# Optimization experiments

Hardware: AMD Instinct MI355X
Metric: run time of the kernel (lower is better)

Reference implementation:

```python
import jax, jax.numpy as jnp
import numpy as np

B_, L, DM = 2, 2048, 1024
DI, N, K, R = 2048, 16, 4, 64  # d_inner, d_state, d_conv, dt_rank


def setup_inputs() -> dict:
    key = jax.random.key(0)
    ks = jax.random.split(key, 8)
    return {
        "x": jax.random.normal(ks[0], (B_, L, DM), jnp.float32),
        "W_in": jax.random.normal(ks[1], (DM, 2 * DI), jnp.float32) * 0.02,
        "w_conv": jax.random.normal(ks[2], (DI, K), jnp.float32) * 0.1,
        "b_conv": jnp.zeros((DI,), jnp.float32),
        "W_x": jax.random.normal(ks[3], (DI, R + 2 * N), jnp.float32) * 0.02,
        "W_dt": jax.random.normal(ks[4], (R, DI), jnp.float32) * 0.02,
        "b_dt": jnp.full((DI,), -4.6, jnp.float32),  # softplus(b_dt) ~ 0.01 dt init
        "A_log": jnp.log(jnp.broadcast_to(jnp.arange(1, N + 1, dtype=jnp.float32), (DI, N))),
        "D": jnp.ones((DI,), jnp.float32),
        "W_out": jax.random.normal(ks[5], (DI, DM), jnp.float32) * 0.02,
        "gamma": jnp.ones((DM,), jnp.float32),
        "beta": jnp.zeros((DM,), jnp.float32),
    }


def reference(x, W_in, w_conv, b_conv, W_x, W_dt, b_dt, A_log, D, W_out, gamma, beta):
    Bb, Ll, Dm = x.shape
    Di, Kk = w_conv.shape
    Nn = A_log.shape[1]
    Rr = W_dt.shape[0]
    # in_proj -> (u, z)
    xz = x @ W_in  # [B,L,2*Di]
    u, z = jnp.split(xz, 2, axis=-1)
    # depthwise causal conv1d (kernel K, left pad K-1) + SiLU
    up = jnp.pad(u, ((0, 0), (Kk - 1, 0), (0, 0)))
    conv = b_conv + sum(up[:, k:k + Ll, :] * w_conv[:, k] for k in range(Kk))
    u = jax.nn.silu(conv)  # [B,L,Di]
    # x_proj -> dt, B, C
    dbc = u @ W_x
    dt, Bm, Cm = dbc[..., :Rr], dbc[..., Rr:Rr + Nn], dbc[..., Rr + Nn:]
    delta = jax.nn.softplus(dt @ W_dt + b_dt)  # [B,L,Di]
    A = -jnp.exp(A_log)  # [Di,N]

    def step(h, inputs):
        d_t, B_t, C_t, u_t = inputs  # [B,Di],[B,N],[B,N],[B,Di]
        dA = jnp.exp(d_t[..., None] * A)            # [B,Di,N]
        h = h * dA + (d_t * u_t)[..., None] * B_t[:, None, :]
        y = jnp.einsum('bdn,bn->bd', h, C_t)
        return h, y

    h0 = jnp.zeros((Bb, Di, Nn), x.dtype)
    _, ys = jax.lax.scan(step, h0, (delta.transpose(1, 0, 2), Bm.transpose(1, 0, 2),
                                    Cm.transpose(1, 0, 2), u.transpose(1, 0, 2)))
    y = ys.transpose(1, 0, 2)        # [B,L,Di]
    y = y + u * D                    # skip term
    y = y * jax.nn.silu(z)           # gate
    out = y @ W_out                  # [B,L,Dm]
    # LayerNorm
    mu = out.mean(-1, keepdims=True)
    var = ((out - mu) ** 2).mean(-1, keepdims=True)
    out = (out - mu) * jax.lax.rsqrt(var + 1e-5) * gamma + beta
    # dropout p=0 -> identity; residual
    return out + x
```

## Files before the change

### kernel.cpp

```cpp
#include <hip/hip_runtime.h>
#include <math.h>

#define L_SEQ 2048
#define DMOD  1024
#define DIN   2048
#define NBATCH 2
#define NTOK  (NBATCH * L_SEQ)
#define NST   16
#define RRANK 64
#define LOG2E 1.44269504088896f

#define GCHUNK 64
#define CLEN   (L_SEQ / GCHUNK)
#define SCHUNK 8
#define NSTAGE (CLEN / SCHUNK)

#define G4_KS   4
#define G4_KC   (2048 / G4_KS)
#define G2_KS   16
#define G2_KC   (2048 / G2_KS)

typedef __attribute__((ext_vector_type(8))) short  short8;
typedef __attribute__((ext_vector_type(4))) float  f32x4;

__device__ __forceinline__ ushort f2bf(float f) {
    unsigned u = __float_as_uint(f);
    u += 0x7fffu + ((u >> 16) & 1u);
    return (ushort)(u >> 16);
}
__device__ __forceinline__ float bf2f(ushort u) {
    return __uint_as_float(((unsigned)u) << 16);
}
__device__ __forceinline__ float fexp2(float x) {
    return __builtin_amdgcn_exp2f(x);
}

__device__ __forceinline__ void gload16(const ushort* g, ushort* l) {
    __builtin_amdgcn_global_load_lds(
        (const __attribute__((address_space(1))) unsigned int*)g,
        (__attribute__((address_space(3))) unsigned int*)l,
        16, 0, 0);
}

__device__ __forceinline__ void cast_body(
    const float* __restrict__ src, ushort* __restrict__ dst, int bid, int tid)
{
    int i = (bid * 256 + tid) * 8;
    float4 a = *(const float4*)(src + i);
    float4 b = *(const float4*)(src + i + 4);
    ushort4 o0 = make_ushort4(f2bf(a.x), f2bf(a.y), f2bf(a.z), f2bf(a.w));
    ushort4 o1 = make_ushort4(f2bf(b.x), f2bf(b.y), f2bf(b.z), f2bf(b.w));
    *(ushort4*)(dst + i)     = o0;
    *(ushort4*)(dst + i + 4) = o1;
}

__device__ __forceinline__ void tcast_body(
    const float* __restrict__ src, ushort* __restrict__ dst,
    int R, int C, int bx, int by, int tid)
{
    __shared__ float t[32][33];
    int tx = tid & 31;
    int ty = tid >> 5;
    int c0 = bx * 32;
    int r0 = by * 32;
    #pragma unroll
    for (int i = 0; i < 4; ++i)
        t[ty + i * 8][tx] = src[(size_t)(r0 + ty + i * 8) * C + c0 + tx];
    __syncthreads();
    #pragma unroll
    for (int i = 0; i < 4; ++i)
        dst[(size_t)(c0 + ty + i * 8) * R + r0 + tx] = f2bf(t[tx][ty + i * 8]);
}

__global__ __launch_bounds__(256) void prep_k(
    const float* __restrict__ x, const float* __restrict__ W_in,
    const float* __restrict__ W_dt, const float* __restrict__ W_x,
    const float* __restrict__ W_out,
    ushort* __restrict__ xb, ushort* __restrict__ Wib,
    ushort* __restrict__ Wdtb, ushort* __restrict__ Wxb,
    ushort* __restrict__ Wob)
{
    int bid = blockIdx.x, tid = threadIdx.x;
    if (bid < 2048) {
        cast_body(x, xb, bid, tid);
    } else if (bid < 6144) {
        int t = bid - 2048;
        tcast_body(W_in, Wib, 1024, 4096, t & 127, t >> 7, tid);
    } else if (bid < 6272) {
        int t = bid - 6144;
        tcast_body(W_dt, Wdtb, 64, 2048, t & 63, t >> 6, tid);
    } else if (bid < 6464) {
        int t = bid - 6272;
        tcast_body(W_x, Wxb, 2048, 96, t % 3, t / 3, tid);
    } else {
        int t = bid - 6464;
        tcast_body(W_out, Wob, 2048, 1024, t & 31, t >> 5, tid);
    }
}

__global__ __launch_bounds__(512, 2) void gemm8p(
    const ushort* __restrict__ A,
    const ushort* __restrict__ Bt,
    ushort* __restrict__ C,
    int K, int kslice, int ldc, size_t zstride)
{
    __shared__ ushort lds[65536];

    const int tid  = threadIdx.x;
    const int wave = tid >> 6;
    const int lane = tid & 63;
    const int wr   = wave >> 2;
    const int wc   = wave & 3;

    const int gx = gridDim.x;
    int flat = blockIdx.y * gx + blockIdx.x;
    const int cpx = (gx * gridDim.y) >> 3;
    flat = (flat & 7) * cpx + (flat >> 3);
    const int bx = flat % gx;
    const int by = flat / gx;
    const int m0 = by * 256;
    const int n0 = bx * 256;
    const int kbeg = blockIdx.z * kslice;
    const int NT   = kslice >> 6;

    const int rr  = tid >> 2;
    const int gsw = ((tid & 3) ^ ((tid >> 3) & 3)) * 8;
    const ushort* a0 = A  + (size_t)(m0 + rr)        * K + kbeg + gsw;
    const ushort* a1 = A  + (size_t)(m0 + 128 + rr)  * K + kbeg + gsw;
    const ushort* b0 = Bt + (size_t)(n0 + rr)        * K + kbeg + gsw;
    const ushort* b1 = Bt + (size_t)(n0 + 128 + rr)  * K + kbeg + gsw;

    #define STAGE_U(op_, ks_, kt_, bf_) do {                                   \
        const int ko_ = (kt_) * 64 + (ks_) * 32;                               \
        ushort* l_ = lds + (bf_) * 32768 + (op_) * 16384 + (ks_) * 8192        \
                         + wave * 512;                                         \
        if ((op_) == 0) { gload16(a0 + ko_, l_); gload16(a1 + ko_, l_ + 4096); }\
        else            { gload16(b0 + ko_, l_); gload16(b1 + ko_, l_ + 4096); }\
    } while (0)

    const int lr  = lane & 15;
    const int swr = ((lane >> 4) ^ ((lr >> 1) & 3)) * 8;

    #define LDA(i_, ks_) (*(const short8*)&lds[buf * 32768 + (ks_) * 8192      \
        + (wr * 128 + (i_) * 16 + lr) * 32 + swr])
    #define LDB(j_, ks_) (*(const short8*)&lds[buf * 32768 + 16384             \
        + (ks_) * 8192 + (wc * 64 + (j_) * 16 + lr) * 32 + swr])

    f32x4 acc[8][4];
    #pragma unroll
    for (int i = 0; i < 8; ++i)
        #pragma unroll
        for (int j = 0; j < 4; ++j)
            acc[i][j] = (f32x4){0.f, 0.f, 0.f, 0.f};

    STAGE_U(0, 0, 0, 0); STAGE_U(1, 0, 0, 0);
    STAGE_U(0, 1, 0, 0); STAGE_U(1, 1, 0, 0);
    asm volatile("s_waitcnt vmcnt(4)" ::: "memory");
    __builtin_amdgcn_s_barrier();

    short8 a_[4], b_[4];

    for (int t = 0; t < NT; ++t) {
        const int buf = t & 1, nb = buf ^ 1;
        const bool st = (t + 1 < NT);

        #pragma unroll
        for (int i = 0; i < 4; ++i) a_[i] = LDA(i, 0);
        #pragma unroll
        for (int j = 0; j < 4; ++j) b_[j] = LDB(j, 0);
        if (st) STAGE_U(0, 0, t + 1, nb);
        __builtin_amdgcn_s_barrier();
        asm volatile("s_waitcnt lgkmcnt(0)" ::: "memory");
        __builtin_amdgcn_sched_barrier(0);
        __builtin_amdgcn_s_setprio(1);
        #pragma unroll
        for (int i = 0; i < 4; ++i)
            #pragma unroll
            for (int j = 0; j < 4; ++j)
                acc[i][j] = __builtin_amdgcn_mfma_f32_16x16x32_bf16(
                    a_[i], b_[j], acc[i][j], 0, 0, 0);
        __builtin_amdgcn_s_setprio(0);
        __builtin_amdgcn_s_barrier();

        #pragma unroll
        for (int i = 0; i < 4; ++i) a_[i] = LDA(4 + i, 0);
        if (st) {
            STAGE_U(1, 0, t + 1, nb);
            asm volatile("s_waitcnt vmcnt(4)" ::: "memory");
        } else {
            asm volatile("s_waitcnt vmcnt(0)" ::: "memory");
        }
        __builtin_amdgcn_s_barrier();
        asm volatile("s_waitcnt lgkmcnt(0)" ::: "memory");
        __builtin_amdgcn_sched_barrier(0);
        __builtin_amdgcn_s_setprio(1);
        #pragma unroll
        for (int i = 0; i < 4; ++i)
            #pragma unroll
            for (int j = 0; j < 4; ++j)
                acc[4 + i][j] = __builtin_amdgcn_mfma_f32_16x16x32_bf16(
                    a_[i], b_[j], acc[4 + i][j], 0, 0, 0);
        __builtin_amdgcn_s_setprio(0);
        __builtin_amdgcn_s_barrier();

        #pragma unroll
        for (int i = 0; i < 4; ++i) a_[i] = LDA(i, 1);
        #pragma unroll
        for (int j = 0; j < 4; ++j) b_[j] = LDB(j, 1);
        if (st) STAGE_U(0, 1, t + 1, nb);
        __builtin_amdgcn_s_barrier();
        asm volatile("s_waitcnt lgkmcnt(0)" ::: "memory");
        __builtin_amdgcn_sched_barrier(0);
        __builtin_amdgcn_s_setprio(1);
        #pragma unroll
        for (int i = 0; i < 4; ++i)
            #pragma unroll
            for (int j = 0; j < 4; ++j)
                acc[i][j] = __builtin_amdgcn_mfma_f32_16x16x32_bf16(
                    a_[i], b_[j], acc[i][j], 0, 0, 0);
        __builtin_amdgcn_s_setprio(0);
        __builtin_amdgcn_s_barrier();

        #pragma unroll
        for (int i = 0; i < 4; ++i) a_[i] = LDA(4 + i, 1);
        if (st) {
            STAGE_U(1, 1, t + 1, nb);
            asm volatile("s_waitcnt vmcnt(4)" ::: "memory");
        }
        __builtin_amdgcn_s_barrier();
        asm volatile("s_waitcnt lgkmcnt(0)" ::: "memory");
        __builtin_amdgcn_sched_barrier(0);
        __builtin_amdgcn_s_setprio(1);
        #pragma unroll
        for (int i = 0; i < 4; ++i)
            #pragma unroll
            for (int j = 0; j < 4; ++j)
                acc[4 + i][j] = __builtin_amdgcn_mfma_f32_16x16x32_bf16(
                    a_[i], b_[j], acc[4 + i][j], 0, 0, 0);
        __builtin_amdgcn_s_setprio(0);
        __builtin_amdgcn_s_barrier();
    }
    #undef STAGE_U
    #undef LDA
    #undef LDB

    ushort* Cp = C + (size_t)blockIdx.z * zstride;
    const int rb = m0 + wr * 128 + ((lane >> 4) << 2);
    const int cb = n0 + wc * 64 + lr;
    #pragma unroll
    for (int i = 0; i < 8; ++i)
        #pragma unroll
        for (int j = 0; j < 4; ++j)
            #pragma unroll
            for (int r = 0; r < 4; ++r)
                Cp[(size_t)(rb + i * 16 + r) * ldc + cb + j * 16] =
                    f2bf(acc[i][j][r]);
}

template<int EPI, int OBF>
__global__ __launch_bounds__(256) void gemm_mfma(
    const ushort* __restrict__ A,
    const ushort* __restrict__ Bt,
    void* __restrict__ Cv,
    int M, int N, int K, int ldc, const float* __restrict__ bias)
{
    __shared__ ushort As[128 * 32];
    __shared__ ushort Bs[128 * 32];

    const int tid  = threadIdx.x;
    const int wave = tid >> 6;
    const int lane = tid & 63;
    const int wm   = (wave & 1) * 64;
    const int wn   = (wave >> 1) * 64;
    const int m0   = blockIdx.y * 128;
    const int n0   = blockIdx.x * 128;

    const int srow = lane >> 2;
    const int sg   = (lane & 3) ^ ((srow >> 1) & 3);
    const ushort* gA0 = A  + (size_t)(m0 + wave * 32 + srow)      * K + sg * 8;
    const ushort* gA1 = A  + (size_t)(m0 + wave * 32 + 16 + srow) * K + sg * 8;
    const ushort* gB0 = Bt + (size_t)(n0 + wave * 32 + srow)      * K + sg * 8;
    const ushort* gB1 = Bt + (size_t)(n0 + wave * 32 + 16 + srow) * K + sg * 8;
    ushort* lA0 = As + (wave * 32)      * 32;
    ushort* lA1 = As + (wave * 32 + 16) * 32;
    ushort* lB0 = Bs + (wave * 32)      * 32;
    ushort* lB1 = Bs + (wave * 32 + 16) * 32;

    const int lrow = lane & 15;
    const int swr  = ((lane >> 4) ^ ((lrow >> 1) & 3)) * 8;

    f32x4 acc[4][4];
    #pragma unroll
    for (int i = 0; i < 4; ++i)
        #pragma unroll
        for (int j = 0; j < 4; ++j)
            acc[i][j] = (f32x4){0.f, 0.f, 0.f, 0.f};

    for (int k0 = 0; k0 < K; k0 += 32) {
        __syncthreads();
        gload16(gA0 + k0, lA0);
        gload16(gA1 + k0, lA1);
        gload16(gB0 + k0, lB0);
        gload16(gB1 + k0, lB1);
        __syncthreads();

        short8 af[4], bfr[4];
        #pragma unroll
        for (int i = 0; i < 4; ++i) {
            af[i]  = *(const short8*)&As[(wm + i * 16 + lrow) * 32 + swr];
            bfr[i] = *(const short8*)&Bs[(wn + i * 16 + lrow) * 32 + swr];
        }
        #pragma unroll
        for (int i = 0; i < 4; ++i)
            #pragma unroll
            for (int j = 0; j < 4; ++j)
                acc[i][j] = __builtin_amdgcn_mfma_f32_16x16x32_bf16(
                    af[i], bfr[j], acc[i][j], 0, 0, 0);
    }

    const int rb = m0 + wm + ((lane >> 4) << 2);
    const int cb = n0 + wn + lrow;

    float bias4[4];
    if (EPI == 1) {
        #pragma unroll
        for (int j = 0; j < 4; ++j) bias4[j] = bias[cb + j * 16];
    }

    #pragma unroll
    for (int i = 0; i < 4; ++i)
        #pragma unroll
        for (int j = 0; j < 4; ++j)
            #pragma unroll
            for (int r = 0; r < 4; ++r) {
                float v = acc[i][j][r];
                int col = cb + j * 16;
                if (EPI == 1) {
                    v += bias4[j];
                    if (v <= 20.f) {
                        float t = fexp2(v * LOG2E);
                        v = __builtin_amdgcn_logf(1.f + t) * (1.f / LOG2E);
                    }
                }
                size_t off = (size_t)(rb + i * 16 + r) * ldc + col;
                if (OBF) ((ushort*)Cv)[off] = f2bf(v);
                else     ((float*)Cv)[off]  = v;
            }
}

__global__ __launch_bounds__(256) void gemm2_mfma(
    const ushort* __restrict__ A,
    const ushort* __restrict__ Bt,
    float* __restrict__ part)
{
    __shared__ ushort As[128 * 32];
    __shared__ ushort Bs[128 * 32];

    const int K = 2048;
    const int tid  = threadIdx.x;
    const int wave = tid >> 6;
    const int lane = tid & 63;
    const int wm   = (wave & 1) * 64;
    const int wn   = (wave >> 1) * 64;
    const int m0   = blockIdx.x * 128;
    const int ks   = blockIdx.z;

    const int srow = lane >> 2;
    const int sg   = (lane & 3) ^ ((srow >> 1) & 3);
    int rB0 = wave * 32 + srow;      if (rB0 > 95) rB0 = 95;
    int rB1 = wave * 32 + 16 + srow; if (rB1 > 95) rB1 = 95;
    const ushort* gA0 = A  + (size_t)(m0 + wave * 32 + srow)      * K + sg * 8;
    const ushort* gA1 = A  + (size_t)(m0 + wave * 32 + 16 + srow) * K + sg * 8;
    const ushort* gB0 = Bt + (size_t)rB0 * K + sg * 8;
    const ushort* gB1 = Bt + (size_t)rB1 * K + sg * 8;
    ushort* lA0 = As + (wave * 32)      * 32;
    ushort* lA1 = As + (wave * 32 + 16) * 32;
    ushort* lB0 = Bs + (wave * 32)      * 32;
    ushort* lB1 = Bs + (wave * 32 + 16) * 32;

    const int lrow = lane & 15;
    const int swr  = ((lane >> 4) ^ ((lrow >> 1) & 3)) * 8;

    f32x4 acc[4][4];
    #pragma unroll
    for (int i = 0; i < 4; ++i)
        #pragma unroll
        for (int j = 0; j < 4; ++j)
            acc[i][j] = (f32x4){0.f, 0.f, 0.f, 0.f};

    const int kbeg = ks * G2_KC, kend = kbeg + G2_KC;
    for (int k0 = kbeg; k0 < kend; k0 += 32) {
        __syncthreads();
        gload16(gA0 + k0, lA0);
        gload16(gA1 + k0, lA1);
        gload16(gB0 + k0, lB0);
        gload16(gB1 + k0, lB1);
        __syncthreads();

        short8 af[4], bfr[4];
        #pragma unroll
        for (int i = 0; i < 4; ++i) {
            af[i]  = *(const short8*)&As[(wm + i * 16 + lrow) * 32 + swr];
            bfr[i] = *(const short8*)&Bs[(wn + i * 16 + lrow) * 32 + swr];
        }
        #pragma unroll
        for (int i = 0; i < 4; ++i)
            #pragma unroll
            for (int j = 0; j < 4; ++j)
                acc[i][j] = __builtin_amdgcn_mfma_f32_16x16x32_bf16(
                    af[i], bfr[j], acc[i][j], 0, 0, 0);
    }

    float* po = part + (size_t)ks * NTOK * 96;
    const int rb = m0 + wm + ((lane >> 4) << 2);
    const int cb = wn + lrow;
    #pragma unroll
    for (int i = 0; i < 4; ++i)
        #pragma unroll
        for (int j = 0; j < 4; ++j) {
            int col = cb + j * 16;
            if (col < 96) {
                #pragma unroll
                for (int r = 0; r < 4; ++r)
                    po[(size_t)(rb + i * 16 + r) * 96 + col] = acc[i][j][r];
            }
        }
}

__global__ __launch_bounds__(256) void gemm2_reduce_dt(
    const float* __restrict__ part, float* __restrict__ dbc,
    ushort* __restrict__ dtb)
{
    int i = (blockIdx.x * 256 + threadIdx.x) * 4;
    float4 s = *(const float4*)(part + i);
    #pragma unroll
    for (int ks = 1; ks < G2_KS; ++ks) {
        float4 v = *(const float4*)(part + (size_t)ks * NTOK * 96 + i);
        s.x += v.x; s.y += v.y; s.z += v.z; s.w += v.w;
    }
    *(float4*)(dbc + i) = s;
    int col = i % 96;
    if (col < RRANK) {
        int row = i / 96;
        ushort* q = dtb + (size_t)row * RRANK + col;
        q[0] = f2bf(s.x); q[1] = f2bf(s.y); q[2] = f2bf(s.z); q[3] = f2bf(s.w);
    }
}

__global__ __launch_bounds__(256) void conv_silu_k(
    const ushort* __restrict__ xzb, const float* __restrict__ w_conv,
    const float* __restrict__ b_conv, ushort* __restrict__ ub)
{
    const int token = blockIdx.x;
    const int d     = threadIdx.x * 8;
    const int t     = token & (L_SEQ - 1);

    float4 w[8];
    const float4* pw = (const float4*)(w_conv + (size_t)d * 4);
    #pragma unroll
    for (int i = 0; i < 8; ++i) w[i] = pw[i];

    float acc[8];
    {
        float4 bc0 = *(const float4*)(b_conv + d);
        float4 bc1 = *(const float4*)(b_conv + d + 4);
        acc[0] = bc0.x; acc[1] = bc0.y; acc[2] = bc0.z; acc[3] = bc0.w;
        acc[4] = bc1.x; acc[5] = bc1.y; acc[6] = bc1.z; acc[7] = bc1.w;
    }

    #pragma unroll
    for (int k = 0; k < 4; ++k) {
        int tt = t - 3 + k;
        if (tt >= 0) {
            short8 v = *(const short8*)(xzb + (size_t)(token - 3 + k) * 4096 + d);
            #pragma unroll
            for (int i = 0; i < 8; ++i)
                acc[i] += bf2f((ushort)v[i]) * (&w[i].x)[k];
        }
    }

    short8 o;
    #pragma unroll
    for (int i = 0; i < 8; ++i) {
        float s = acc[i] / (1.f + __expf(-acc[i]));
        o[i] = (short)f2bf(s);
    }
    *(short8*)(ub + (size_t)token * DIN + d) = o;
}

__global__ __launch_bounds__(64) void scan_part1(
    const float* __restrict__ dlt,
    const ushort* __restrict__ ub,
    const float* __restrict__ dbc,
    const float* __restrict__ A_log,
    float* __restrict__ c_out,
    float* __restrict__ dsum_out)
{
    int chunk = blockIdx.x & 63;
    int dg    = (blockIdx.x >> 6) & 31;
    int b     = blockIdx.x >> 11;
    int tid   = threadIdx.x;
    int d     = dg * 64 + tid;

    __shared__ float sB[SCHUNK][16];

    float Al[NST];
    const float4* pA = (const float4*)(A_log + (size_t)d * NST);
    #pragma unroll
    for (int q = 0; q < 4; ++q) {
        float4 a = pA[q];
        Al[q*4+0] = -__expf(a.x) * LOG2E;
        Al[q*4+1] = -__expf(a.y) * LOG2E;
        Al[q*4+2] = -__expf(a.z) * LOG2E;
        Al[q*4+3] = -__expf(a.w) * LOG2E;
    }

    float h[NST];
    #pragma unroll
    for (int n = 0; n < NST; ++n) h[n] = 0.f;
    float dsum = 0.f;

    const size_t tokbase = (size_t)b * L_SEQ + (size_t)chunk * CLEN;
    const float*  pD = dlt + tokbase * 2048 + d;
    const ushort* pU = ub  + tokbase * 2048 + d;
    const float*  pB = dbc + tokbase * 96 + RRANK;

    float rd[2][SCHUNK], ru[2][SCHUNK], rb[2][2];

    #pragma unroll
    for (int i = 0; i < SCHUNK; ++i) {
        rd[0][i] = pD[(size_t)i * 2048];
        ru[0][i] = bf2f(pU[(size_t)i * 2048]);
    }
    #pragma unroll
    for (int i = 0; i < 2; ++i) {
        int e = i * 64 + tid;
        rb[0][i] = pB[(size_t)(e >> 4) * 96 + (e & 15)];
    }

    #pragma unroll
    for (int st = 0; st < NSTAGE; ++st) {
        const int cur = st & 1, nxt = cur ^ 1;
        #pragma unroll
        for (int i = 0; i < 2; ++i) {
            int e = i * 64 + tid;
            sB[e >> 4][e & 15] = rb[cur][i];
        }
        if (st + 1 < NSTAGE) {
            const size_t to = (size_t)(st + 1) * SCHUNK;
            #pragma unroll
            for (int i = 0; i < SCHUNK; ++i) {
                rd[nxt][i] = pD[(to + i) * 2048];
                ru[nxt][i] = bf2f(pU[(to + i) * 2048]);
            }
            #pragma unroll
            for (int i = 0; i < 2; ++i) {
                int e = i * 64 + tid;
                rb[nxt][i] = pB[(to + (e >> 4)) * 96 + (e & 15)];
            }
        }
        #pragma unroll
        for (int s = 0; s < SCHUNK; ++s) {
            float delta = rd[cur][s];
            float du    = delta * ru[cur][s];
            dsum += delta;
            #pragma unroll
            for (int q = 0; q < 4; ++q) {
                float4 bq = *(const float4*)&sB[s][q * 4];
                h[q*4+0] = h[q*4+0] * fexp2(delta * Al[q*4+0]) + du * bq.x;
                h[q*4+1] = h[q*4+1] * fexp2(delta * Al[q*4+1]) + du * bq.y;
                h[q*4+2] = h[q*4+2] * fexp2(delta * Al[q*4+2]) + du * bq.z;
                h[q*4+3] = h[q*4+3] * fexp2(delta * Al[q*4+3]) + du * bq.w;
            }
        }
    }

    size_t base = (((size_t)b * DIN + d) * GCHUNK + chunk) * NST;
    #pragma unroll
    for (int q = 0; q < 4; ++q)
        *(float4*)&c_out[base + q * 4] = make_float4(h[q*4], h[q*4+1], h[q*4+2], h[q*4+3]);
    dsum_out[((size_t)b * DIN + d) * GCHUNK + chunk] = dsum;
}

__global__ __launch_bounds__(256) void scan_part2(
    float* __restrict__ cbuf,
    const float* __restrict__ dsum_in,
    const float* __restrict__ A_log)
{
    int idx = blockIdx.x * 256 + threadIdx.x;
    int n   = idx & 15;
    int d   = (idx >> 4) & (DIN - 1);
    int b   = idx >> 15;

    float Al = -__expf(A_log[(size_t)d * NST + n]) * LOG2E;
    size_t cb = ((size_t)b * DIN + d) * GCHUNK;

    float h = 0.f;
    for (int ch = 0; ch < GCHUNK; ++ch) {
        size_t o = (cb + ch) * NST + n;
        float c  = cbuf[o];
        float dA = fexp2(Al * dsum_in[cb + ch]);
        cbuf[o]  = h;
        h = h * dA + c;
    }
}

__global__ __launch_bounds__(64) void scan_part3(
    const float* __restrict__ dlt,
    const ushort* __restrict__ xzb,
    ushort* __restrict__ ub,
    const float* __restrict__ dbc,
    const float* __restrict__ A_log,
    const float* __restrict__ Dp,
    const float* __restrict__ h_start)
{
    int chunk = blockIdx.x & 63;
    int dg    = (blockIdx.x >> 6) & 31;
    int b     = blockIdx.x >> 11;
    int tid   = threadIdx.x;
    int d     = dg * 64 + tid;

    __shared__ float sBC[SCHUNK][32];

    float Al[NST];
    const float4* pA = (const float4*)(A_log + (size_t)d * NST);
    #pragma unroll
    for (int q = 0; q < 4; ++q) {
        float4 a = pA[q];
        Al[q*4+0] = -__expf(a.x) * LOG2E;
        Al[q*4+1] = -__expf(a.y) * LOG2E;
        Al[q*4+2] = -__expf(a.z) * LOG2E;
        Al[q*4+3] = -__expf(a.w) * LOG2E;
    }
    float Dd = Dp[d];

    float h[NST];
    size_t hb = (((size_t)b * DIN + d) * GCHUNK + chunk) * NST;
    #pragma unroll
    for (int q = 0; q < 4; ++q) {
        float4 v = *(const float4*)&h_start[hb + q * 4];
        h[q*4] = v.x; h[q*4+1] = v.y; h[q*4+2] = v.z; h[q*4+3] = v.w;
    }

    const size_t tokbase = (size_t)b * L_SEQ + (size_t)chunk * CLEN;
    const float*  pD = dlt + tokbase * 2048 + d;
    const ushort* pZ = xzb + tokbase * 4096 + 2048 + d;
    ushort*       pU = ub  + tokbase * 2048 + d;
    const float*  pB = dbc + tokbase * 96 + RRANK;

    float rd[2][SCHUNK], ru[2][SCHUNK], rz[2][SCHUNK], rb[2][4];

    #pragma unroll
    for (int i = 0; i < SCHUNK; ++i) {
        rd[0][i] = pD[(size_t)i * 2048];
        ru[0][i] = bf2f(pU[(size_t)i * 2048]);
        rz[0][i] = bf2f(pZ[(size_t)i * 4096]);
    }
    #pragma unroll
    for (int i = 0; i < 4; ++i) {
        int e = i * 64 + tid;
        rb[0][i] = pB[(size_t)(e >> 5) * 96 + (e & 31)];
    }

    #pragma unroll
    for (int st = 0; st < NSTAGE; ++st) {
        const int cur = st & 1, nxt = cur ^ 1;
        #pragma unroll
        for (int i = 0; i < 4; ++i) {
            int e = i * 64 + tid;
            sBC[e >> 5][e & 31] = rb[cur][i];
        }
        if (st + 1 < NSTAGE) {
            const size_t to = (size_t)(st + 1) * SCHUNK;
            #pragma unroll
            for (int i = 0; i < SCHUNK; ++i) {
                rd[nxt][i] = pD[(to + i) * 2048];
                ru[nxt][i] = bf2f(pU[(to + i) * 2048]);
                rz[nxt][i] = bf2f(pZ[(to + i) * 4096]);
            }
            #pragma unroll
            for (int i = 0; i < 4; ++i) {
                int e = i * 64 + tid;
                rb[nxt][i] = pB[(to + (e >> 5)) * 96 + (e & 31)];
            }
        }
        #pragma unroll
        for (int s = 0; s < SCHUNK; ++s) {
            float delta = rd[cur][s];
            float u     = ru[cur][s];
            float du    = delta * u;
            float y = 0.f;
            #pragma unroll
            for (int q = 0; q < 4; ++q) {
                float4 bq = *(const float4*)&sBC[s][q * 4];
                float4 cq = *(const float4*)&sBC[s][16 + q * 4];
                h[q*4+0] = h[q*4+0] * fexp2(delta * Al[q*4+0]) + du * bq.x; y += h[q*4+0] * cq.x;
                h[q*4+1] = h[q*4+1] * fexp2(delta * Al[q*4+1]) + du * bq.y; y += h[q*4+1] * cq.y;
                h[q*4+2] = h[q*4+2] * fexp2(delta * Al[q*4+2]) + du * bq.z; y += h[q*4+2] * cq.z;
                h[q*4+3] = h[q*4+3] * fexp2(delta * Al[q*4+3]) + du * bq.w; y += h[q*4+3] * cq.w;
            }
            float z  = rz[cur][s];
            float sz = z / (1.f + __expf(-z));
            pU[((size_t)st * SCHUNK + s) * 2048] = f2bf((y + u * Dd) * sz);
        }
    }
}

__global__ __launch_bounds__(256) void ln4_k(
    const ushort* __restrict__ part,
    const float* __restrict__ x,
    const float* __restrict__ gamma, const float* __restrict__ beta,
    float* __restrict__ out)
{
    int row = blockIdx.x;
    int tid = threadIdx.x;
    const size_t off = (size_t)row * DMOD + tid * 4;

    float4 v = {0.f, 0.f, 0.f, 0.f};
    #pragma unroll
    for (int ks = 0; ks < G4_KS; ++ks) {
        ushort4 p = *(const ushort4*)(part + (size_t)ks * NTOK * DMOD + off);
        v.x += bf2f(p.x); v.y += bf2f(p.y); v.z += bf2f(p.z); v.w += bf2f(p.w);
    }

    float s  = v.x + v.y + v.z + v.w;
    float s2 = v.x * v.x + v.y * v.y + v.z * v.z + v.w * v.w;
    #pragma unroll
    for (int off2 = 32; off2 > 0; off2 >>= 1) {
        s  += __shfl_down(s, off2);
        s2 += __shfl_down(s2, off2);
    }
    __shared__ float ws[4], ws2[4];
    int wave = tid >> 6, lane = tid & 63;
    if (lane == 0) { ws[wave] = s; ws2[wave] = s2; }
    __syncthreads();
    if (tid == 0) {
        float ts = 0.f, ts2 = 0.f;
        #pragma unroll
        for (int w = 0; w < 4; ++w) { ts += ws[w]; ts2 += ws2[w]; }
        ws[0] = ts; ws2[0] = ts2;
    }
    __syncthreads();
    float mu  = ws[0] * (1.f / DMOD);
    float var = ws2[0] * (1.f / DMOD) - mu * mu;
    float rs  = rsqrtf(var + 1e-5f);

    float4 g  = ((const float4*)gamma)[tid];
    float4 be = ((const float4*)beta)[tid];
    float4 xr = *(const float4*)(x + off);
    float4 o;
    o.x = (v.x - mu) * rs * g.x + be.x + xr.x;
    o.y = (v.y - mu) * rs * g.y + be.y + xr.y;
    o.z = (v.z - mu) * rs * g.z + be.z + xr.z;
    o.w = (v.w - mu) * rs * g.w + be.w + xr.w;
    *(float4*)(out + off) = o;
}

extern "C" void kernel_launch(void* const* d_in, const int* in_sizes, int n_in,
                              void* d_out, int out_size, void* d_ws, size_t ws_size,
                              hipStream_t stream)
{
    const float* x      = (const float*)d_in[0];
    const float* W_in   = (const float*)d_in[1];
    const float* w_conv = (const float*)d_in[2];
    const float* b_conv = (const float*)d_in[3];
    const float* W_x    = (const float*)d_in[4];
    const float* W_dt   = (const float*)d_in[5];
    const float* b_dt   = (const float*)d_in[6];
    const float* A_log  = (const float*)d_in[7];
    const float* Dp     = (const float*)d_in[8];
    const float* W_out  = (const float*)d_in[9];
    const float* gamma  = (const float*)d_in[10];
    const float* beta   = (const float*)d_in[11];
    float* out = (float*)d_out;

    char* ws = (char*)d_ws;
    const size_t MB = 1024 * 1024;
    ushort* xzb   = (ushort*)(ws);
    ushort* ub    = (ushort*)(ws + 32 * MB);
    float*  dlt   = (float*)(ws + 48 * MB);
    float*  dbc   = (float*)(ws + 80 * MB);
    ushort* Wdtb  = (ushort*)(ws + 81 * MB + 512 * 1024);
    ushort* Wxb   = (ushort*)(ws + 81 * MB + 768 * 1024);
    float*  dsum  = (float*)(ws + 82 * MB + 256 * 1024);
    float*  c_buf = (float*)(ws + 84 * MB);
    ushort* xb    = (ushort*)(ws + 84 * MB);
    ushort* Wib   = (ushort*)(ws + 92 * MB);
    float*  g2part = (float*)(ws + 84 * MB);
    ushort* dtb   = (ushort*)(ws + 108 * MB);
    ushort* Wob   = (ushort*)(ws + 109 * MB);
    ushort* g4part = (ushort*)(ws + 48 * MB);

    dim3 blk(256);

    prep_k<<<dim3(8512), blk, 0, stream>>>(x, W_in, W_dt, W_x, W_out,
                                           xb, Wib, Wdtb, Wxb, Wob);
    gemm8p<<<dim3(16, 16, 1), dim3(512), 0, stream>>>(
        xb, Wib, xzb, 1024, 1024, 4096, 0);
    conv_silu_k<<<dim3(NTOK), blk, 0, stream>>>(xzb, w_conv, b_conv, ub);
    gemm2_mfma<<<dim3(32, 1, G2_KS), blk, 0, stream>>>(ub, Wxb, g2part);
    gemm2_reduce_dt<<<dim3(NTOK * 96 / 4 / 256), blk, 0, stream>>>(g2part, dbc, dtb);
    gemm_mfma<1, 0><<<dim3(16, 32), blk, 0, stream>>>(
        dtb, Wdtb, dlt, 4096, 2048, 64, 2048, b_dt);
    scan_part1<<<dim3(NBATCH * 32 * GCHUNK), dim3(64), 0, stream>>>(
        dlt, ub, dbc, A_log, c_buf, dsum);
    scan_part2<<<dim3(NBATCH * DIN * NST / 256), blk, 0, stream>>>(
        c_buf, dsum, A_log);
    scan_part3<<<dim3(NBATCH * 32 * GCHUNK), dim3(64), 0, stream>>>(
        dlt, xzb, ub, dbc, A_log, Dp, c_buf);
    gemm8p<<<dim3(4, 16, G4_KS), dim3(512), 0, stream>>>(
        ub, Wob, g4part, 2048, G4_KC, DMOD, (size_t)NTOK * DMOD);
    ln4_k<<<dim3(NTOK), blk, 0, stream>>>(g4part, x, gamma, beta, out);
}
```

Measured before the change: 315.3 us.

## Split in_proj into separate u/z buffers and double scan chunk count

The in_proj GEMM is split into two launches that write u and z into separate contiguous bf16 buffers. The conv and scan_part3 kernels then read with a 2048 stride instead of 4096. The number of scan chunks per sequence is raised from 64 to 128, which doubles the scan_part1/part3 grid for more parallelism but lengthens the serial carry pass in scan_part2 and enlarges the carry buffer. The workspace layout is repacked to fit. Each of the two GEMM launches has half the blocks of the original fused launch, which may underfill the GPU.

```diff
diff --git a/kernel.cpp b/kernel.cpp
--- a/kernel.cpp
+++ b/kernel.cpp
@@ -10,7 +10,7 @@
 #define RRANK 64
 #define LOG2E 1.44269504088896f
 
-#define GCHUNK 64
+#define GCHUNK 128
 #define CLEN   (L_SEQ / GCHUNK)
 #define SCHUNK 8
 #define NSTAGE (CLEN / SCHUNK)
@@ -448,7 +448,7 @@
 }
 
 __global__ __launch_bounds__(256) void conv_silu_k(
-    const ushort* __restrict__ xzb, const float* __restrict__ w_conv,
+    const ushort* __restrict__ up, const float* __restrict__ w_conv,
     const float* __restrict__ b_conv, ushort* __restrict__ ub)
 {
     const int token = blockIdx.x;
@@ -472,7 +472,7 @@
     for (int k = 0; k < 4; ++k) {
         int tt = t - 3 + k;
         if (tt >= 0) {
-            short8 v = *(const short8*)(xzb + (size_t)(token - 3 + k) * 4096 + d);
+            short8 v = *(const short8*)(up + (size_t)(token - 3 + k) * 2048 + d);
             #pragma unroll
             for (int i = 0; i < 8; ++i)
                 acc[i] += bf2f((ushort)v[i]) * (&w[i].x)[k];
@@ -496,9 +496,9 @@
     float* __restrict__ c_out,
     float* __restrict__ dsum_out)
 {
-    int chunk = blockIdx.x & 63;
-    int dg    = (blockIdx.x >> 6) & 31;
-    int b     = blockIdx.x >> 11;
+    int chunk = blockIdx.x & (GCHUNK - 1);
+    int dg    = (blockIdx.x / GCHUNK) & 31;
+    int b     = blockIdx.x / (GCHUNK * 32);
     int tid   = threadIdx.x;
     int d     = dg * 64 + tid;
 
@@ -607,16 +607,16 @@
 
 __global__ __launch_bounds__(64) void scan_part3(
     const float* __restrict__ dlt,
-    const ushort* __restrict__ xzb,
+    const ushort* __restrict__ zb,
     ushort* __restrict__ ub,
     const float* __restrict__ dbc,
     const float* __restrict__ A_log,
     const float* __restrict__ Dp,
     const float* __restrict__ h_start)
 {
-    int chunk = blockIdx.x & 63;
-    int dg    = (blockIdx.x >> 6) & 31;
-    int b     = blockIdx.x >> 11;
+    int chunk = blockIdx.x & (GCHUNK - 1);
+    int dg    = (blockIdx.x / GCHUNK) & 31;
+    int b     = blockIdx.x / (GCHUNK * 32);
     int tid   = threadIdx.x;
     int d     = dg * 64 + tid;
 
@@ -644,7 +644,7 @@
 
     const size_t tokbase = (size_t)b * L_SEQ + (size_t)chunk * CLEN;
     const float*  pD = dlt + tokbase * 2048 + d;
-    const ushort* pZ = xzb + tokbase * 4096 + 2048 + d;
+    const ushort* pZ = zb  + tokbase * 2048 + d;
     ushort*       pU = ub  + tokbase * 2048 + d;
     const float*  pB = dbc + tokbase * 96 + RRANK;
 
@@ -654,7 +654,7 @@
     for (int i = 0; i < SCHUNK; ++i) {
         rd[0][i] = pD[(size_t)i * 2048];
         ru[0][i] = bf2f(pU[(size_t)i * 2048]);
-        rz[0][i] = bf2f(pZ[(size_t)i * 4096]);
+        rz[0][i] = bf2f(pZ[(size_t)i * 2048]);
     }
     #pragma unroll
     for (int i = 0; i < 4; ++i) {
@@ -676,7 +676,7 @@
             for (int i = 0; i < SCHUNK; ++i) {
                 rd[nxt][i] = pD[(to + i) * 2048];
                 ru[nxt][i] = bf2f(pU[(to + i) * 2048]);
-                rz[nxt][i] = bf2f(pZ[(to + i) * 4096]);
+                rz[nxt][i] = bf2f(pZ[(to + i) * 2048]);
             }
             #pragma unroll
             for (int i = 0; i < 4; ++i) {
@@ -776,28 +776,31 @@
 
     char* ws = (char*)d_ws;
     const size_t MB = 1024 * 1024;
-    ushort* xzb   = (ushort*)(ws);
-    ushort* ub    = (ushort*)(ws + 32 * MB);
-    float*  dlt   = (float*)(ws + 48 * MB);
-    float*  dbc   = (float*)(ws + 80 * MB);
-    ushort* Wdtb  = (ushort*)(ws + 81 * MB + 512 * 1024);
-    ushort* Wxb   = (ushort*)(ws + 81 * MB + 768 * 1024);
-    float*  dsum  = (float*)(ws + 82 * MB + 256 * 1024);
-    float*  c_buf = (float*)(ws + 84 * MB);
-    ushort* xb    = (ushort*)(ws + 84 * MB);
-    ushort* Wib   = (ushort*)(ws + 92 * MB);
-    float*  g2part = (float*)(ws + 84 * MB);
-    ushort* dtb   = (ushort*)(ws + 108 * MB);
-    ushort* Wob   = (ushort*)(ws + 109 * MB);
-    ushort* g4part = (ushort*)(ws + 48 * MB);
+    ushort* zb     = (ushort*)(ws);
+    ushort* ub     = (ushort*)(ws + 16 * MB);
+    float*  dlt    = (float*)(ws + 32 * MB);
+    float*  dbc    = (float*)(ws + 64 * MB);
+    ushort* Wdtb   = (ushort*)(ws + 65 * MB + 512 * 1024);
+    ushort* Wxb    = (ushort*)(ws + 65 * MB + 768 * 1024);
+    ushort* dtb    = (ushort*)(ws + 66 * MB + 128 * 1024);
+    float*  dsum   = (float*)(ws + 67 * MB);
+    ushort* Wob    = (ushort*)(ws + 69 * MB);
+    float*  c_buf  = (float*)(ws + 73 * MB);
+    ushort* xb     = (ushort*)(ws + 73 * MB);
+    ushort* Wib    = (ushort*)(ws + 81 * MB);
+    ushort* ub_pre = (ushort*)(ws + 89 * MB);
+    float*  g2part = (float*)(ws + 73 * MB);
+    ushort* g4part = (ushort*)(ws + 32 * MB);
 
     dim3 blk(256);
 
     prep_k<<<dim3(8512), blk, 0, stream>>>(x, W_in, W_dt, W_x, W_out,
                                            xb, Wib, Wdtb, Wxb, Wob);
-    gemm8p<<<dim3(16, 16, 1), dim3(512), 0, stream>>>(
-        xb, Wib, xzb, 1024, 1024, 4096, 0);
-    conv_silu_k<<<dim3(NTOK), blk, 0, stream>>>(xzb, w_conv, b_conv, ub);
+    gemm8p<<<dim3(8, 16, 1), dim3(512), 0, stream>>>(
+        xb, Wib, ub_pre, 1024, 1024, 2048, 0);
+    gemm8p<<<dim3(8, 16, 1), dim3(512), 0, stream>>>(
+        xb, Wib + (size_t)2048 * 1024, zb, 1024, 1024, 2048, 0);
+    conv_silu_k<<<dim3(NTOK), blk, 0, stream>>>(ub_pre, w_conv, b_conv, ub);
     gemm2_mfma<<<dim3(32, 1, G2_KS), blk, 0, stream>>>(ub, Wxb, g2part);
     gemm2_reduce_dt<<<dim3(NTOK * 96 / 4 / 256), blk, 0, stream>>>(g2part, dbc, dtb);
     gemm_mfma<1, 0><<<dim3(16, 32), blk, 0, stream>>>(
@@ -807,7 +810,7 @@
     scan_part2<<<dim3(NBATCH * DIN * NST / 256), blk, 0, stream>>>(
         c_buf, dsum, A_log);
     scan_part3<<<dim3(NBATCH * 32 * GCHUNK), dim3(64), 0, stream>>>(
-        dlt, xzb, ub, dbc, A_log, Dp, c_buf);
+        dlt, zb, ub, dbc, A_log, Dp, c_buf);
     gemm8p<<<dim3(4, 16, G4_KS), dim3(512), 0, stream>>>(
         ub, Wob, g4part, 2048, G4_KC, DMOD, (size_t)NTOK * DMOD);
     ln4_k<<<dim3(NTOK), blk, 0, stream>>>(g4part, x, gamma, beta, out);
```

Result: slower. 339.9 us (+7.8%).
